# Optimization experiments

Hardware: AMD Instinct MI355X
Metric: run time of the kernel (lower is better)

Reference implementation:

```python
import jax, jax.numpy as jnp
import numpy as np
from jax import lax

B, C, H, W = 2, 256, 64, 64
KC, RD = C // 8, C // 16  # key_channels=32, GatherExcite rd_channels=16
EPS = 1e-5


def setup_inputs() -> dict:
    key = jax.random.key(0)
    ks = jax.random.split(key, 17)
    s = 0.05
    n = lambda k, shp: jax.random.normal(k, shp, jnp.float32) * s
    return {
        "x": jax.random.normal(ks[0], (B, C, H, W), jnp.float32),
        "Wq": n(ks[1], (KC, C)),
        "Wk": n(ks[2], (KC, C)),
        "Wv": n(ks[3], (C, C)),
        "Wb1": n(ks[4], (KC, C)),
        "Wb2": n(ks[5], (KC, C)),
        "w_gb": jax.random.normal(ks[6], (), jnp.float32),  # 1x1 conv on 1-channel bias map
        "ge_w1": n(ks[7], (RD, C)),
        "ge_b1": jnp.zeros((RD,), jnp.float32),
        "ge_w2": n(ks[8], (C, RD)),
        "ge_b2": jnp.zeros((C,), jnp.float32),
        "Wo": n(ks[9], (C, C)),
        "bn_scale": jnp.ones((C,), jnp.float32),
        "bn_bias": jnp.zeros((C,), jnp.float32),
        "bn_mean": jax.random.normal(ks[10], (C,), jnp.float32) * 0.01,
        "bn_var": jnp.ones((C,), jnp.float32),
        "gamma": jax.random.normal(ks[11], (), jnp.float32) * 0.1,
    }


def _conv1x1(t, w):  # t: [B,Cin,H,W], w: [Cout,Cin]
    return jnp.einsum('bchw,oc->bohw', t, w)


def reference(x, Wq, Wk, Wv, Wb1, Wb2, w_gb, ge_w1, ge_b1, ge_w2, ge_b2,
              Wo, bn_scale, bn_bias, bn_mean, bn_var, gamma):
    b, c, h, w = x.shape
    hw = h * w

    # GatherExcite (extent=0, use_mlp=True, gate=sigmoid): global mean -> ConvMlp -> sigmoid gate
    m = x.mean(axis=(2, 3), keepdims=True)                     # [B,C,1,1]
    g = jax.nn.relu(_conv1x1(m, ge_w1) + ge_b1[None, :, None, None])
    g = _conv1x1(g, ge_w2) + ge_b2[None, :, None, None]
    key_in = x * jax.nn.sigmoid(g)                             # [B,C,H,W]

    value = _conv1x1(x, Wv).reshape(b, c, hw).transpose(0, 2, 1)   # [B,HW,C]
    query = _conv1x1(x, Wq).reshape(b, KC, hw).transpose(0, 2, 1)  # [B,HW,Kc]
    key_f = _conv1x1(key_in, Wk).reshape(b, KC, hw)                # [B,Kc,HW]

    sim = jnp.einsum('bnk,bkm->bnm', query, key_f)                 # [B,HW,HW]

    # bias branch (dropout is identity at eval)
    b1 = jax.nn.relu(_conv1x1(x, Wb1)).reshape(b, KC, hw)          # [B,Kc,HW]
    b2 = jax.nn.relu(_conv1x1(x, Wb2)).reshape(b, KC, hw)          # [B,Kc,HW]
    bias = jnp.einsum('bkn,bkm->bnm', b1, b2)                      # [B,HW,HW]

    # AvgPool2d(k=3, s=1, pad=1, count_include_pad=True) on [B,1,HW,HW]
    pooled = lax.reduce_window(bias[:, None], 0.0, lax.add,
                               (1, 1, 3, 3), (1, 1, 1, 1),
                               [(0, 0), (0, 0), (1, 1), (1, 1)]) / 9.0
    bias_map = jax.nn.sigmoid(w_gb * pooled)[:, 0]                 # [B,HW,HW]

    attn = jax.nn.softmax(sim * bias_map, axis=-1)                 # [B,HW,HW]
    ctx = jnp.einsum('bnm,bmc->bnc', attn, value)                  # [B,HW,C]
    ctx = ctx.transpose(0, 2, 1).reshape(b, c, h, w)

    # W: conv1x1 -> BatchNorm (inference) -> ReLU
    y = _conv1x1(ctx, Wo)
    y = (y - bn_mean[None, :, None, None]) * (bn_scale / jnp.sqrt(bn_var + EPS))[None, :, None, None] \
        + bn_bias[None, :, None, None]
    y = jax.nn.relu(y)

    return gamma * y + x
```

## Files before the change

kernel.cpp:

```cpp
#include <hip/hip_runtime.h>
#include <hip/hip_bf16.h>

typedef __bf16 bf16;
typedef __bf16 v8bf __attribute__((ext_vector_type(8)));
typedef __bf16 v4bf __attribute__((ext_vector_type(4)));
typedef float v4f __attribute__((ext_vector_type(4)));

#define HW 4096
#define CH 256
#define KC 32
#define RD 16
#define NB 2
#define BNEPS 1e-5f
#define LOG2E 1.4426950408889634f

__device__ __forceinline__ float fexp2(float x) {
#if __has_builtin(__builtin_amdgcn_exp2f)
  return __builtin_amdgcn_exp2f(x);
#else
  return exp2f(x);
#endif
}
__device__ __forceinline__ float frcp(float x) {
#if __has_builtin(__builtin_amdgcn_rcpf)
  return __builtin_amdgcn_rcpf(x);
#else
  return 1.f / x;
#endif
}

__device__ __forceinline__ int xcd_swz(int bid, int nwg) {
  return (bid & 7) * (nwg >> 3) + (bid >> 3);
}

#define OFF_QT     0u
#define OFF_KT     524288u
#define OFF_BS1    1048576u
#define OFF_BS2    1572864u
#define OFF_VF     2097152u
#define OFF_B1R    6291456u
#define OFF_B2R    6815744u
#define OFF_PACC   7340032u
#define OFF_PL     40894464u
#define OFF_WOBF   41156608u
#define OFF_XBT    41287680u
#define OFF_WALL   45481984u
#define OFF_MPART  45875200u

__global__ __launch_bounds__(256) void k_prep(const float* __restrict__ x,
    bf16* __restrict__ xbt, float* __restrict__ mpart) {
  __shared__ __align__(16) float ts[64][68];
  const int blk = blockIdx.x;
  const int b  = blk >> 8;
  const int id = blk & 255;
  const int ct = id >> 6, nt = id & 63;
  const int c0 = ct * 64, n0 = nt * 64;
  const int t = threadIdx.x;
  const int crow = t >> 2, nch = (t & 3) * 16;
  const float* xp = x + ((size_t)(b * CH + c0 + crow)) * HW + n0 + nch;
  #pragma unroll
  for (int i = 0; i < 4; ++i)
    *(v4f*)&ts[crow][nch + i * 4] = *(const v4f*)(xp + i * 4);
  __syncthreads();
  {
    float p = 0.f;
    #pragma unroll
    for (int j = 0; j < 16; ++j) p += ts[crow][nch + j];
    p += __shfl_xor(p, 1);
    p += __shfl_xor(p, 2);
    if ((t & 3) == 0) mpart[(size_t)(b * CH + c0 + crow) * 64 + nt] = p;
  }
  const int nl = t >> 2, cc0 = (t & 3) * 16;
  bf16* dst = xbt + ((size_t)(b * HW + n0 + nl)) * CH + c0 + cc0;
  v8bf o0, o1;
  #pragma unroll
  for (int j = 0; j < 8; ++j) { o0[j] = (bf16)ts[cc0 + j][nl]; o1[j] = (bf16)ts[cc0 + 8 + j][nl]; }
  *(v8bf*)dst = o0;
  *(v8bf*)(dst + 8) = o1;
}

__global__ __launch_bounds__(256) void k_pack(
    const float* __restrict__ mpart,
    const float* __restrict__ gw1, const float* __restrict__ gb1,
    const float* __restrict__ gw2, const float* __restrict__ gb2,
    const float* __restrict__ Wq, const float* __restrict__ Wk,
    const float* __restrict__ Wb1, const float* __restrict__ Wb2,
    const float* __restrict__ Wv, const float* __restrict__ Wo,
    bf16* __restrict__ wall, bf16* __restrict__ wo_bf) {
  __shared__ float ms[CH];
  __shared__ float hid[RD];
  const int blk = blockIdx.x;
  const int t = threadIdx.x;
  if (blk >= 768) {
    int i = (blk - 768) * 256 + t;
    wo_bf[i] = (bf16)Wo[i];
    return;
  }
  const int b = blk / 384, row = blk % 384;
  float v;
  if (row < 32)       v = Wq[row * CH + t] * LOG2E;
  else if (row < 64) {
    float m = 0.f;
    const float* mp = mpart + (size_t)(b * CH + t) * 64;
    #pragma unroll
    for (int j = 0; j < 64; ++j) m += mp[j];
    ms[t] = m * (1.0f / HW);
    __syncthreads();
    if (t < RD) {
      float a = gb1[t];
      for (int c = 0; c < CH; ++c) a += gw1[t * CH + c] * ms[c];
      hid[t] = fmaxf(a, 0.f);
    }
    __syncthreads();
    float a = gb2[t];
    #pragma unroll
    for (int r = 0; r < RD; ++r) a += gw2[t * RD + r] * hid[r];
    float s = 1.f / (1.f + __expf(-a));
    v = Wk[(row - 32) * CH + t] * s;
  }
  else if (row < 96)  v = Wb1[(row - 64) * CH + t];
  else if (row < 128) v = Wb2[(row - 96) * CH + t];
  else                v = Wv[(row - 128) * CH + t];
  wall[((size_t)b * 384 + row) * CH + t] = (bf16)v;
}

__global__ __launch_bounds__(256, 4) void k_proj(
    const bf16* __restrict__ xbt, const bf16* __restrict__ wall,
    bf16* __restrict__ qt, bf16* __restrict__ kt,
    bf16* __restrict__ b1r, bf16* __restrict__ b2r, bf16* __restrict__ vfg) {
  __shared__ __align__(16) bf16 xs[16][264];
  __shared__ __align__(16) bf16 tr[4][16][24];
  const int blk = blockIdx.x;
  const int b = blk >> 8, nt = blk & 255;
  const int n0 = nt * 16;
  const int t = threadIdx.x;
  {
    const int row = t >> 4, c0 = (t & 15) * 16;
    const bf16* src = xbt + ((size_t)(b * HW + n0 + row)) * CH + c0;
    *(v8bf*)&xs[row][c0] = *(const v8bf*)src;
    *(v8bf*)&xs[row][c0 + 8] = *(const v8bf*)(src + 8);
  }
  __syncthreads();
  const int w = t >> 6, lane = t & 63, cl = lane & 15, kh = lane >> 4;
  const v4f vzero = {0.f, 0.f, 0.f, 0.f};
  v4f acc[6] = {vzero, vzero, vzero, vzero, vzero, vzero};
  const bf16* wb = wall + ((size_t)b * 384 + w * 96) * CH;
  for (int kk = 0; kk < 8; ++kk) {
    v8bf bx = *(const v8bf*)&xs[cl][kk * 32 + kh * 8];
    #pragma unroll
    for (int j = 0; j < 6; ++j) {
      v8bf af = *(const v8bf*)(wb + (size_t)(j * 16 + cl) * CH + kk * 32 + kh * 8);
      acc[j] = __builtin_amdgcn_mfma_f32_16x16x32_bf16(af, bx, acc[j], 0, 0, 0);
    }
  }
  const int n = n0 + cl;
  #pragma unroll
  for (int j = 0; j < 6; ++j) {
    const int o0 = w * 96 + j * 16;
    if (o0 < 128) {
      const bool rel = (o0 >= 64);
      v4bf pk;
      #pragma unroll
      for (int r = 0; r < 4; ++r) {
        float v = acc[j][r];
        if (rel) v = fmaxf(v, 0.f);
        pk[r] = (bf16)v;
      }
      const int seg = o0 >> 5;
      bf16* base = seg == 0 ? qt : seg == 1 ? kt : seg == 2 ? b1r : b2r;
      *(v4bf*)&base[((size_t)b * HW + n) * KC + (o0 & 31) + kh * 4] = pk;
    } else {
      #pragma unroll
      for (int r = 0; r < 4; ++r) tr[w][kh * 4 + r][cl] = (bf16)acc[j][r];
      asm volatile("s_waitcnt lgkmcnt(0)" ::: "memory");
      __builtin_amdgcn_sched_barrier(0);
      if (lane < 32) {
        const int clf = lane & 15, khl = (lane >> 4) & 1;
        const int khf = (((n0 >> 4) & 1) << 1) + khl;
        const int s = n0 >> 5, f = (o0 - 128) >> 4;
        v8bf d = *(const v8bf*)&tr[w][clf][khl * 8];
        *(v8bf*)&vfg[((((size_t)b * 128 + s) * 16 + f) * 64 + khf * 16 + clf) * 8] = d;
      }
    }
  }
}

__global__ __launch_bounds__(256) void k_pool(const bf16* __restrict__ b1r,
    const bf16* __restrict__ b2r, const float* __restrict__ wgb,
    bf16* __restrict__ bs1, bf16* __restrict__ bs2) {
  int i = blockIdx.x * 256 + threadIdx.x;
  int n = (i >> 5) & (HW - 1);
  float a = (float)b1r[i], c = (float)b2r[i];
  if (n > 0)      { a += (float)b1r[i - KC]; c += (float)b2r[i - KC]; }
  if (n < HW - 1) { a += (float)b1r[i + KC]; c += (float)b2r[i + KC]; }
  const float ws = -LOG2E * wgb[0] * (1.f / 9.f);
  bs1[i] = (bf16)(a * ws);
  bs2[i] = (bf16)c;
}

__global__ __launch_bounds__(256, 4) void k_attn(
    const bf16* __restrict__ qtg, const bf16* __restrict__ ktg,
    const bf16* __restrict__ bs1g, const bf16* __restrict__ bs2g,
    const bf16* __restrict__ vfg,
    bf16* __restrict__ pacc, float* __restrict__ pl) {
  __shared__ __align__(16) bf16 kbuf[2][32][40];
  __shared__ __align__(16) bf16 bbuf[2][32][40];
  __shared__ __align__(16) bf16 plds[2][64][40];
  __shared__ __align__(16) bf16 escr[4][16][72];
  const int blk = xcd_swz(blockIdx.x, 1024);
  const int rt  = blk >> 3;
  const int os  = blk & 7;
  const int b   = rt >> 6;
  const int row0 = (rt & 63) * 64;
  const int t = threadIdx.x;
  const int w = t >> 6;
  const int lane = t & 63;
  const int cl = lane & 15, kh = lane >> 4;
  const int kb = os * 512;
  const v4f vzero = {0.f, 0.f, 0.f, 0.f};
  const size_t qoff = ((size_t)(b * HW + row0 + w * 16 + cl)) * KC + kh * 8;
  const v8bf qf  = *(const v8bf*)(qtg + qoff);
  const v8bf b1f = *(const v8bf*)(bs1g + qoff);
  const bf16* kt = ktg + (size_t)b * HW * KC;
  const bf16* b2 = bs2g + (size_t)b * HW * KC;
  const bf16* vfb = vfg + ((((size_t)b * 128 + (kb >> 5)) * 16) + w * 4) * 512 + (size_t)lane * 8;
  const int sr = (t >> 2) & 31, sl = (t & 3) * 8;
  const bf16* sbase = (t < 128) ? kt : b2;
  bf16* sd0 = (t < 128) ? &kbuf[0][sr][sl] : &bbuf[0][sr][sl];
  bf16* sd1 = (t < 128) ? &kbuf[1][sr][sl] : &bbuf[1][sr][sl];

  *(v8bf*)sd0 = *(const v8bf*)(sbase + (size_t)(kb + sr) * KC + sl);
  __syncthreads();

  v4f acc[16];
  #pragma unroll
  for (int f = 0; f < 16; ++f) acc[f] = vzero;
  float psum = 0.f;

  for (int s = 0; s < 16; ++s) {
    const int m0 = kb + s * 32;
    const int pb = s & 1;
    v8bf pr;
    if (s < 15)
      pr = *(const v8bf*)(sbase + (size_t)(m0 + 32 + sr) * KC + sl);
    #pragma unroll
    for (int cb = 0; cb < 2; ++cb) {
      v8bf kf  = *(const v8bf*)&kbuf[pb][cb * 16 + cl][kh * 8];
      v8bf b2f = *(const v8bf*)&bbuf[pb][cb * 16 + cl][kh * 8];
      v4f sim = __builtin_amdgcn_mfma_f32_16x16x32_bf16(kf,  qf,  vzero, 0, 0, 0);
      v4f bia = __builtin_amdgcn_mfma_f32_16x16x32_bf16(b2f, b1f, vzero, 0, 0, 0);
      v4bf pk;
      #pragma unroll
      for (int r = 0; r < 4; ++r) {
        float bm = frcp(1.f + fexp2(bia[r]));
        float pv = fexp2(sim[r] * bm);
        psum += pv;
        pk[r] = (bf16)pv;
      }
      *(v4bf*)&plds[pb][w * 16 + cl][cb * 16 + kh * 4] = pk;
    }
    if (s < 15) {
      bf16* sd = pb ? sd0 : sd1;
      *(v8bf*)sd = pr;
    }
    __syncthreads();
    const bf16* vs = vfb + (size_t)s * 8192;
    v8bf vf0 = *(const v8bf*)(vs);
    v8bf vf1 = *(const v8bf*)(vs + 512);
    v8bf vf2 = *(const v8bf*)(vs + 1024);
    v8bf vf3 = *(const v8bf*)(vs + 1536);
    #pragma unroll
    for (int rg = 0; rg < 4; ++rg) {
      v8bf pa = *(const v8bf*)&plds[pb][rg * 16 + cl][kh * 8];
      acc[rg * 4 + 0] = __builtin_amdgcn_mfma_f32_16x16x32_bf16(pa, vf0, acc[rg * 4 + 0], 0, 0, 0);
      acc[rg * 4 + 1] = __builtin_amdgcn_mfma_f32_16x16x32_bf16(pa, vf1, acc[rg * 4 + 1], 0, 0, 0);
      acc[rg * 4 + 2] = __builtin_amdgcn_mfma_f32_16x16x32_bf16(pa, vf2, acc[rg * 4 + 2], 0, 0, 0);
      acc[rg * 4 + 3] = __builtin_amdgcn_mfma_f32_16x16x32_bf16(pa, vf3, acc[rg * 4 + 3], 0, 0, 0);
    }
  }
  __syncthreads();

  {
    float s2 = psum;
    s2 += __shfl_xor(s2, 16);
    s2 += __shfl_xor(s2, 32);
    if (kh == 0) pl[blk * 64 + w * 16 + cl] = s2;
  }
  bf16* po = pacc + (size_t)blk * 64 * CH;
  for (int rg = 0; rg < 4; ++rg) {
    #pragma unroll
    for (int f = 0; f < 4; ++f)
      #pragma unroll
      for (int r = 0; r < 4; ++r)
        escr[w][kh * 4 + r][f * 16 + cl] = (bf16)acc[rg * 4 + f][r];
    asm volatile("s_waitcnt lgkmcnt(0)" ::: "memory");
    __builtin_amdgcn_sched_barrier(0);
    #pragma unroll
    for (int it = 0; it < 2; ++it) {
      int row = lane >> 2, chunk = it * 4 + (lane & 3);
      v8bf d = *(const v8bf*)&escr[w][row][chunk * 8];
      *(v8bf*)&po[(size_t)(rg * 16 + row) * CH + w * 64 + chunk * 8] = d;
    }
  }
}

__global__ __launch_bounds__(256) void k_outc(
    const bf16* __restrict__ pacc, const float* __restrict__ pl,
    const bf16* __restrict__ wo,
    const float* __restrict__ bns, const float* __restrict__ bnb,
    const float* __restrict__ bnm, const float* __restrict__ bnv,
    const float* __restrict__ gamma, const float* __restrict__ x,
    float* __restrict__ out) {
  __shared__ __align__(16) bf16 cs[16][264];
  const int blk = xcd_swz(blockIdx.x, 512);
  const int n0g = blk * 16;
  const int b   = n0g >> 12;
  const int n0  = n0g & (HW - 1);
  const int t = threadIdx.x;
  const int base = (blk >> 2) * 8;
  {
    const int r16 = t >> 4;
    const int ch0 = (t & 15) * 16;
    const int rl = (blk & 3) * 16 + r16;
    float den = 0.f;
    #pragma unroll
    for (int s = 0; s < 8; ++s) den += pl[(base + s) * 64 + rl];
    const float inv = 1.f / den;
    float sum[16];
    #pragma unroll
    for (int j = 0; j < 16; ++j) sum[j] = 0.f;
    #pragma unroll
    for (int s = 0; s < 8; ++s) {
      const bf16* pp = &pacc[((size_t)(base + s) * 64 + rl) * CH + ch0];
      v8bf p0 = *(const v8bf*)pp;
      v8bf p1 = *(const v8bf*)(pp + 8);
      #pragma unroll
      for (int j = 0; j < 8; ++j) { sum[j] += (float)p0[j]; sum[8 + j] += (float)p1[j]; }
    }
    v8bf o0, o1;
    #pragma unroll
    for (int j = 0; j < 8; ++j) {
      o0[j] = (bf16)(sum[j] * inv);
      o1[j] = (bf16)(sum[8 + j] * inv);
    }
    *(v8bf*)&cs[r16][ch0] = o0;
    *(v8bf*)&cs[r16][ch0 + 8] = o1;
  }
  __syncthreads();
  const int w = t >> 6, lane = t & 63, cl = lane & 15, kh = lane >> 4;
  const v4f vzero = {0.f, 0.f, 0.f, 0.f};
  v8bf a[8];
  #pragma unroll
  for (int kk = 0; kk < 8; ++kk)
    a[kk] = *(const v8bf*)&cs[cl][kk * 32 + kh * 8];
  v4f acc[4] = {vzero, vzero, vzero, vzero};
  #pragma unroll
  for (int kk = 0; kk < 8; ++kk)
    #pragma unroll
    for (int cg = 0; cg < 4; ++cg) {
      v8bf bfr = *(const v8bf*)(wo + (size_t)(w * 64 + cg * 16 + cl) * CH + kk * 32 + kh * 8);
      acc[cg] = __builtin_amdgcn_mfma_f32_16x16x32_bf16(a[kk], bfr, acc[cg], 0, 0, 0);
    }
  const float g = gamma[0];
  #pragma unroll
  for (int cg = 0; cg < 4; ++cg) {
    int o = w * 64 + cg * 16 + cl;
    float isc = bns[o] / sqrtf(bnv[o] + BNEPS);
    float mu = bnm[o], bb = bnb[o];
    size_t oi = ((size_t)b * CH + o) * HW + n0 + kh * 4;
    v4f xv = *(const v4f*)&x[oi];
    v4f ov;
    #pragma unroll
    for (int r = 0; r < 4; ++r) {
      float v = (acc[cg][r] - mu) * isc + bb;
      v = fmaxf(v, 0.f);
      ov[r] = g * v + xv[r];
    }
    *(v4f*)&out[oi] = ov;
  }
}

extern "C" void kernel_launch(void* const* d_in, const int* in_sizes, int n_in,
                              void* d_out, int out_size, void* d_ws, size_t ws_size,
                              hipStream_t stream) {
  const float* x    = (const float*)d_in[0];
  const float* Wq   = (const float*)d_in[1];
  const float* Wk   = (const float*)d_in[2];
  const float* Wv   = (const float*)d_in[3];
  const float* Wb1  = (const float*)d_in[4];
  const float* Wb2  = (const float*)d_in[5];
  const float* wgb  = (const float*)d_in[6];
  const float* gw1  = (const float*)d_in[7];
  const float* gb1  = (const float*)d_in[8];
  const float* gw2  = (const float*)d_in[9];
  const float* gb2  = (const float*)d_in[10];
  const float* Wo   = (const float*)d_in[11];
  const float* bns  = (const float*)d_in[12];
  const float* bnb  = (const float*)d_in[13];
  const float* bnm  = (const float*)d_in[14];
  const float* bnv  = (const float*)d_in[15];
  const float* gam  = (const float*)d_in[16];

  char* ws = (char*)d_ws;
  bf16* qt    = (bf16*)(ws + OFF_QT);
  bf16* kt    = (bf16*)(ws + OFF_KT);
  bf16* bs1   = (bf16*)(ws + OFF_BS1);
  bf16* bs2   = (bf16*)(ws + OFF_BS2);
  bf16* vfg   = (bf16*)(ws + OFF_VF);
  bf16* b1r   = (bf16*)(ws + OFF_B1R);
  bf16* b2r   = (bf16*)(ws + OFF_B2R);
  bf16* pacc  = (bf16*)(ws + OFF_PACC);
  float* plv  = (float*)(ws + OFF_PL);
  bf16* wobf  = (bf16*)(ws + OFF_WOBF);
  bf16* xbt   = (bf16*)(ws + OFF_XBT);
  bf16* wall  = (bf16*)(ws + OFF_WALL);
  float* mprt = (float*)(ws + OFF_MPART);
  float* out  = (float*)d_out;

  hipLaunchKernelGGL(k_prep, dim3(512),  dim3(256), 0, stream, x, xbt, mprt);
  hipLaunchKernelGGL(k_pack, dim3(1024), dim3(256), 0, stream, mprt, gw1, gb1, gw2, gb2,
                     Wq, Wk, Wb1, Wb2, Wv, Wo, wall, wobf);
  hipLaunchKernelGGL(k_proj, dim3(512),  dim3(256), 0, stream, xbt, wall, qt, kt, b1r, b2r, vfg);
  hipLaunchKernelGGL(k_pool, dim3(NB * HW * KC / 256), dim3(256), 0, stream, b1r, b2r, wgb, bs1, bs2);
  hipLaunchKernelGGL(k_attn, dim3(1024), dim3(256), 0, stream, qt, kt, bs1, bs2, vfg, pacc, plv);
  hipLaunchKernelGGL(k_outc, dim3(512),  dim3(256), 0, stream, pacc, plv, wobf, bns, bnb, bnm, bnv, gam, x, out);
}
```

Measured before the change: 80.73 us.

## Retile attention to 32 query rows by 1024-key splits, halving partial outputs

Changes the attention work decomposition from 64 query rows by 8 key splits of 512 to 32 query rows by 4 key splits of 1024. Each wave now computes logits for its own 16-key slice across both row groups, and processes 64 keys per step. The partial-context buffer and the combine kernel shrink by half, since only 4 partials per row are written and read. The cost is fewer rows per block, so each V fragment is reused across only two row groups instead of four, and a shared-memory reduction is added for the row sums.

Result: slower. 93.66 us (+16.0%).

```diff
diff --git a/kernel.cpp b/kernel.cpp
--- a/kernel.cpp
+++ b/kernel.cpp
@@ -41,11 +41,11 @@
 #define OFF_B1R    6291456u
 #define OFF_B2R    6815744u
 #define OFF_PACC   7340032u
-#define OFF_PL     40894464u
-#define OFF_WOBF   41156608u
-#define OFF_XBT    41287680u
-#define OFF_WALL   45481984u
-#define OFF_MPART  45875200u
+#define OFF_PL     24117248u
+#define OFF_WOBF   24248320u
+#define OFF_XBT    24379392u
+#define OFF_WALL   28573696u
+#define OFF_MPART  28966912u
 
 __global__ __launch_bounds__(256) void k_prep(const float* __restrict__ x,
     bf16* __restrict__ xbt, float* __restrict__ mpart) {
@@ -203,91 +203,111 @@
     const bf16* __restrict__ bs1g, const bf16* __restrict__ bs2g,
     const bf16* __restrict__ vfg,
     bf16* __restrict__ pacc, float* __restrict__ pl) {
-  __shared__ __align__(16) bf16 kbuf[2][32][40];
-  __shared__ __align__(16) bf16 bbuf[2][32][40];
-  __shared__ __align__(16) bf16 plds[2][64][40];
+  __shared__ __align__(16) bf16 kbuf[2][64][40];
+  __shared__ __align__(16) bf16 bbuf[2][64][40];
+  __shared__ __align__(16) bf16 plds[2][32][72];
   __shared__ __align__(16) bf16 escr[4][16][72];
+  __shared__ float psh[4][32];
   const int blk = xcd_swz(blockIdx.x, 1024);
-  const int rt  = blk >> 3;
-  const int os  = blk & 7;
-  const int b   = rt >> 6;
-  const int row0 = (rt & 63) * 64;
+  const int rt  = blk >> 2;
+  const int os  = blk & 3;
+  const int b   = rt >> 7;
+  const int row0 = (rt & 127) * 32;
   const int t = threadIdx.x;
   const int w = t >> 6;
   const int lane = t & 63;
   const int cl = lane & 15, kh = lane >> 4;
-  const int kb = os * 512;
+  const int kb = os * 1024;
   const v4f vzero = {0.f, 0.f, 0.f, 0.f};
-  const size_t qoff = ((size_t)(b * HW + row0 + w * 16 + cl)) * KC + kh * 8;
-  const v8bf qf  = *(const v8bf*)(qtg + qoff);
-  const v8bf b1f = *(const v8bf*)(bs1g + qoff);
   const bf16* kt = ktg + (size_t)b * HW * KC;
   const bf16* b2 = bs2g + (size_t)b * HW * KC;
+  v8bf qf[2], b1f[2];
+  #pragma unroll
+  for (int rg = 0; rg < 2; ++rg) {
+    const size_t qoff = ((size_t)(b * HW + row0 + rg * 16 + cl)) * KC + kh * 8;
+    qf[rg]  = *(const v8bf*)(qtg + qoff);
+    b1f[rg] = *(const v8bf*)(bs1g + qoff);
+  }
   const bf16* vfb = vfg + ((((size_t)b * 128 + (kb >> 5)) * 16) + w * 4) * 512 + (size_t)lane * 8;
-  const int sr = (t >> 2) & 31, sl = (t & 3) * 8;
+  const int sr = (t >> 1) & 63, sl = (t & 1) * 16;
   const bf16* sbase = (t < 128) ? kt : b2;
   bf16* sd0 = (t < 128) ? &kbuf[0][sr][sl] : &bbuf[0][sr][sl];
   bf16* sd1 = (t < 128) ? &kbuf[1][sr][sl] : &bbuf[1][sr][sl];
 
-  *(v8bf*)sd0 = *(const v8bf*)(sbase + (size_t)(kb + sr) * KC + sl);
-  __syncthreads();
-
-  v4f acc[16];
-  #pragma unroll
-  for (int f = 0; f < 16; ++f) acc[f] = vzero;
-  float psum = 0.f;
+  {
+    const bf16* sp = sbase + (size_t)(kb + sr) * KC + sl;
+    *(v8bf*)sd0 = *(const v8bf*)sp;
+    *(v8bf*)(sd0 + 8) = *(const v8bf*)(sp + 8);
+  }
+  __syncthreads();
+
+  v4f acc[8];
+  #pragma unroll
+  for (int f = 0; f < 8; ++f) acc[f] = vzero;
+  float psum[2] = {0.f, 0.f};
 
   for (int s = 0; s < 16; ++s) {
-    const int m0 = kb + s * 32;
+    const int m0 = kb + s * 64;
     const int pb = s & 1;
-    v8bf pr;
-    if (s < 15)
-      pr = *(const v8bf*)(sbase + (size_t)(m0 + 32 + sr) * KC + sl);
-    #pragma unroll
-    for (int cb = 0; cb < 2; ++cb) {
-      v8bf kf  = *(const v8bf*)&kbuf[pb][cb * 16 + cl][kh * 8];
-      v8bf b2f = *(const v8bf*)&bbuf[pb][cb * 16 + cl][kh * 8];
-      v4f sim = __builtin_amdgcn_mfma_f32_16x16x32_bf16(kf,  qf,  vzero, 0, 0, 0);
-      v4f bia = __builtin_amdgcn_mfma_f32_16x16x32_bf16(b2f, b1f, vzero, 0, 0, 0);
+    v8bf pr0, pr1;
+    if (s < 15) {
+      const bf16* sp = sbase + (size_t)(m0 + 64 + sr) * KC + sl;
+      pr0 = *(const v8bf*)sp;
+      pr1 = *(const v8bf*)(sp + 8);
+    }
+    #pragma unroll
+    for (int rg = 0; rg < 2; ++rg) {
+      v8bf kf  = *(const v8bf*)&kbuf[pb][w * 16 + cl][kh * 8];
+      v8bf b2f = *(const v8bf*)&bbuf[pb][w * 16 + cl][kh * 8];
+      v4f sim = __builtin_amdgcn_mfma_f32_16x16x32_bf16(kf,  qf[rg],  vzero, 0, 0, 0);
+      v4f bia = __builtin_amdgcn_mfma_f32_16x16x32_bf16(b2f, b1f[rg], vzero, 0, 0, 0);
       v4bf pk;
       #pragma unroll
       for (int r = 0; r < 4; ++r) {
         float bm = frcp(1.f + fexp2(bia[r]));
         float pv = fexp2(sim[r] * bm);
-        psum += pv;
+        psum[rg] += pv;
         pk[r] = (bf16)pv;
       }
-      *(v4bf*)&plds[pb][w * 16 + cl][cb * 16 + kh * 4] = pk;
+      *(v4bf*)&plds[pb][rg * 16 + cl][w * 16 + kh * 4] = pk;
     }
     if (s < 15) {
       bf16* sd = pb ? sd0 : sd1;
-      *(v8bf*)sd = pr;
+      *(v8bf*)sd = pr0;
+      *(v8bf*)(sd + 8) = pr1;
     }
     __syncthreads();
-    const bf16* vs = vfb + (size_t)s * 8192;
-    v8bf vf0 = *(const v8bf*)(vs);
-    v8bf vf1 = *(const v8bf*)(vs + 512);
-    v8bf vf2 = *(const v8bf*)(vs + 1024);
-    v8bf vf3 = *(const v8bf*)(vs + 1536);
-    #pragma unroll
-    for (int rg = 0; rg < 4; ++rg) {
-      v8bf pa = *(const v8bf*)&plds[pb][rg * 16 + cl][kh * 8];
-      acc[rg * 4 + 0] = __builtin_amdgcn_mfma_f32_16x16x32_bf16(pa, vf0, acc[rg * 4 + 0], 0, 0, 0);
-      acc[rg * 4 + 1] = __builtin_amdgcn_mfma_f32_16x16x32_bf16(pa, vf1, acc[rg * 4 + 1], 0, 0, 0);
-      acc[rg * 4 + 2] = __builtin_amdgcn_mfma_f32_16x16x32_bf16(pa, vf2, acc[rg * 4 + 2], 0, 0, 0);
-      acc[rg * 4 + 3] = __builtin_amdgcn_mfma_f32_16x16x32_bf16(pa, vf3, acc[rg * 4 + 3], 0, 0, 0);
-    }
-  }
-  __syncthreads();
-
-  {
-    float s2 = psum;
+    const bf16* vs = vfb + (size_t)(s * 2) * 8192;
+    v8bf vf[2][4];
+    #pragma unroll
+    for (int ks = 0; ks < 2; ++ks)
+      #pragma unroll
+      for (int f = 0; f < 4; ++f)
+        vf[ks][f] = *(const v8bf*)(vs + (size_t)ks * 8192 + f * 512);
+    #pragma unroll
+    for (int rg = 0; rg < 2; ++rg)
+      #pragma unroll
+      for (int ks = 0; ks < 2; ++ks) {
+        v8bf pa = *(const v8bf*)&plds[pb][rg * 16 + cl][ks * 32 + kh * 8];
+        #pragma unroll
+        for (int f = 0; f < 4; ++f)
+          acc[rg * 4 + f] = __builtin_amdgcn_mfma_f32_16x16x32_bf16(pa, vf[ks][f], acc[rg * 4 + f], 0, 0, 0);
+      }
+  }
+  __syncthreads();
+
+  #pragma unroll
+  for (int rg = 0; rg < 2; ++rg) {
+    float s2 = psum[rg];
     s2 += __shfl_xor(s2, 16);
     s2 += __shfl_xor(s2, 32);
-    if (kh == 0) pl[blk * 64 + w * 16 + cl] = s2;
-  }
-  bf16* po = pacc + (size_t)blk * 64 * CH;
-  for (int rg = 0; rg < 4; ++rg) {
+    if (kh == 0) psh[w][rg * 16 + cl] = s2;
+  }
+  __syncthreads();
+  if (t < 32)
+    pl[blk * 32 + t] = psh[0][t] + psh[1][t] + psh[2][t] + psh[3][t];
+  bf16* po = pacc + (size_t)blk * 32 * CH;
+  for (int rg = 0; rg < 2; ++rg) {
     #pragma unroll
     for (int f = 0; f < 4; ++f)
       #pragma unroll
@@ -317,21 +337,21 @@
   const int b   = n0g >> 12;
   const int n0  = n0g & (HW - 1);
   const int t = threadIdx.x;
-  const int base = (blk >> 2) * 8;
+  const int base = (blk >> 1) * 4;
   {
     const int r16 = t >> 4;
     const int ch0 = (t & 15) * 16;
-    const int rl = (blk & 3) * 16 + r16;
+    const int rl = (blk & 1) * 16 + r16;
     float den = 0.f;
     #pragma unroll
-    for (int s = 0; s < 8; ++s) den += pl[(base + s) * 64 + rl];
+    for (int s = 0; s < 4; ++s) den += pl[(base + s) * 32 + rl];
     const float inv = 1.f / den;
     float sum[16];
     #pragma unroll
     for (int j = 0; j < 16; ++j) sum[j] = 0.f;
     #pragma unroll
-    for (int s = 0; s < 8; ++s) {
-      const bf16* pp = &pacc[((size_t)(base + s) * 64 + rl) * CH + ch0];
+    for (int s = 0; s < 4; ++s) {
+      const bf16* pp = &pacc[((size_t)(base + s) * 32 + rl) * CH + ch0];
       v8bf p0 = *(const v8bf*)pp;
       v8bf p1 = *(const v8bf*)(pp + 8);
       #pragma unroll
```
